# Kernel optimization log

Measured on AMD Instinct MI355X. Metric: run time of the kernel, lower is better.

Reference implementation:

```python
import jax, jax.numpy as jnp
import numpy as np

N_NODES = 100000
FEAT = 256
EMBED = 128
K = 10          # sampled neighbors per node (num_sample)
E = 4096        # edge batch
NUM_CLASSES = 2


def setup_inputs() -> dict:
    key = jax.random.key(0)
    ks = jax.random.split(key, 6)
    edges = jax.random.randint(ks[0], (E, 2), 0, N_NODES)
    neigh_idx = jax.random.randint(ks[1], (N_NODES, K), 0, N_NODES)
    features = jax.random.normal(ks[2], (N_NODES, FEAT), dtype=jnp.float32)
    W1 = jax.random.normal(ks[3], (EMBED, FEAT), dtype=jnp.float32) * (FEAT ** -0.5)
    W2 = jax.random.normal(ks[4], (EMBED, EMBED), dtype=jnp.float32) * (EMBED ** -0.5)
    Wc = jax.random.normal(ks[5], (NUM_CLASSES, EMBED), dtype=jnp.float32) * (EMBED ** -0.5)
    return {"edges": edges, "neigh_idx": neigh_idx, "features": features,
            "W1": W1, "W2": W2, "Wc": Wc}


def reference(edges, neigh_idx, features, W1, W2, Wc):
    # 2-layer GraphSage-style encoder (gcn mean aggregation), batched over E edges.
    idx2 = neigh_idx[edges]              # [E,2,K]   1-hop neighbors of edge endpoints
    idx1 = neigh_idx[idx2]               # [E,2,K,K] 2-hop neighbors
    # layer 1: mean of raw features over 2-hop neighbor sets, then linear + relu
    f1 = jnp.mean(features[idx1], axis=3)                 # [E,2,K,FEAT]
    h1 = jax.nn.relu(jnp.einsum('epkf,df->epkd', f1, W1)) # [E,2,K,EMBED]
    # layer 2: mean over 1-hop neighbors, then linear (last encoder: no relu)
    h1m = jnp.mean(h1, axis=2)                            # [E,2,EMBED]
    h2 = jnp.einsum('epd,gd->epg', h1m, W2)               # [E,2,EMBED]
    # edge pooling ('mean'): average the two endpoint embeddings
    pooled = 0.5 * (h2[:, 0] + h2[:, 1])                  # [E,EMBED]
    # classifier: weight.mm(embeds).t()
    return pooled @ Wc.T                                  # [E,NUM_CLASSES]
```

## Files before the change

### kernel.cpp

```cpp
#include <hip/hip_runtime.h>
#include <hip/hip_bf16.h>


typedef __bf16 bf16x8 __attribute__((ext_vector_type(8)));
typedef float f32x4 __attribute__((ext_vector_type(4)));

#define FEAT 256
#define EMB  128
#define KNB  10

__device__ inline unsigned short f2b(float f) {
  unsigned int u = __float_as_uint(f);
  unsigned int r = (u + 0x7fffu + ((u >> 16) & 1u)) >> 16;
  return (unsigned short)r;
}
__device__ inline float b2f(unsigned short s) {
  return __uint_as_float(((unsigned int)s) << 16);
}


__global__ void cvt_w1(const float* __restrict__ W1, unsigned short* __restrict__ w1b) {
  int i = blockIdx.x * 256 + threadIdx.x;
  if (i < EMB * FEAT) w1b[i] = f2b(W1[i]);
}

__global__ void make_m2(const float* __restrict__ W2, const float* __restrict__ Wc,
                        float* __restrict__ M2) {
  int t = threadIdx.x;
  int c = t >> 7, d = t & 127;
  float s = 0.f;
  for (int g = 0; g < EMB; ++g) s += Wc[c * EMB + g] * W2[g * EMB + d];
  M2[t] = s;
}


__global__ __launch_bounds__(512, 4) void gemm_z(
    const float* __restrict__ feat, const unsigned short* __restrict__ w1b,
    unsigned short* __restrict__ z, int M) {
  __shared__ unsigned short As[64][FEAT + 8];

  const int wid  = threadIdx.x >> 6;
  const int lane = threadIdx.x & 63;
  const int m0   = blockIdx.x * 64;

  bf16x8 bfrag[8];
  {
    const int col = wid * 16 + (lane & 15);
    const int kof = (lane >> 4) * 8;
#pragma unroll
    for (int kk = 0; kk < 8; ++kk)
      bfrag[kk] = *reinterpret_cast<const bf16x8*>(&w1b[col * FEAT + kk * 32 + kof]);
  }

  const float4* f4 = reinterpret_cast<const float4*>(feat);
  for (int i = threadIdx.x; i < 64 * 64; i += 512) {
    int r = i >> 6, c4 = i & 63;
    int row = m0 + r;
    float4 v = make_float4(0.f, 0.f, 0.f, 0.f);
    if (row < M) v = f4[(size_t)row * 64 + c4];
    ushort4 b;
    b.x = f2b(v.x); b.y = f2b(v.y); b.z = f2b(v.z); b.w = f2b(v.w);
    *reinterpret_cast<ushort4*>(&As[r][c4 * 4]) = b;
  }
  __syncthreads();

  f32x4 acc[4] = {};
  const int arow = lane & 15;
  const int kof  = (lane >> 4) * 8;
#pragma unroll
  for (int mt = 0; mt < 4; ++mt) {
#pragma unroll
    for (int kk = 0; kk < 8; ++kk) {
      bf16x8 a = *reinterpret_cast<const bf16x8*>(&As[mt * 16 + arow][kk * 32 + kof]);
      acc[mt] = __builtin_amdgcn_mfma_f32_16x16x32_bf16(a, bfrag[kk], acc[mt], 0, 0, 0);
    }
  }

  const int col = wid * 16 + (lane & 15);
#pragma unroll
  for (int mt = 0; mt < 4; ++mt) {
    int rbase = m0 + mt * 16 + (lane >> 4) * 4;
#pragma unroll
    for (int r = 0; r < 4; ++r) {
      int row = rbase + r;
      if (row < M) z[(size_t)row * EMB + col] = f2b(acc[mt][r]);
    }
  }
}


__global__ __launch_bounds__(128) void aggregate(
    const int* __restrict__ edges, const int* __restrict__ nidx,
    const unsigned short* __restrict__ z, const float* __restrict__ M2,
    float* __restrict__ out, int E) {
  __shared__ int s_idx1[2 * KNB * KNB];
  __shared__ int s_idx2[2 * KNB];
  __shared__ float pm[EMB];

  const int e = blockIdx.x;
  const int t = threadIdx.x;

  if (t < 2 * KNB) {
    int v = edges[e * 2 + t / KNB];
    s_idx2[t] = nidx[(size_t)v * KNB + (t % KNB)];
  }
  __syncthreads();
  for (int i = t; i < 2 * KNB * KNB; i += 128)
    s_idx1[i] = nidx[(size_t)s_idx2[i / KNB] * KNB + (i % KNB)];
  __syncthreads();

  float pooled = 0.f;
#pragma unroll
  for (int p = 0; p < 2; ++p) {
    float h = 0.f;
#pragma unroll
    for (int k = 0; k < KNB; ++k) {
      float a = 0.f;
#pragma unroll
      for (int j = 0; j < KNB; ++j) {
        int u = s_idx1[p * 100 + k * KNB + j];
        a += b2f(z[(size_t)u * EMB + t]);
      }
      h += fmaxf(a * 0.1f, 0.f);
    }
    pooled += h * 0.1f * 0.5f;
  }

  pm[t] = pooled;
  __syncthreads();
  if (t < 64) {
    float s0 = pm[t] * M2[t]       + pm[t + 64] * M2[t + 64];
    float s1 = pm[t] * M2[EMB + t] + pm[t + 64] * M2[EMB + t + 64];
#pragma unroll
    for (int off = 32; off > 0; off >>= 1) {
      s0 += __shfl_down(s0, off);
      s1 += __shfl_down(s1, off);
    }
    if (t == 0) { out[e * 2 + 0] = s0; out[e * 2 + 1] = s1; }
  }
}


extern "C" void kernel_launch(void* const* d_in, const int* in_sizes, int n_in,
                              void* d_out, int out_size, void* d_ws, size_t ws_size,
                              hipStream_t stream) {
  const int*   edges = (const int*)d_in[0];
  const int*   nidx  = (const int*)d_in[1];
  const float* feat  = (const float*)d_in[2];
  const float* W1    = (const float*)d_in[3];
  const float* W2    = (const float*)d_in[4];
  const float* Wc    = (const float*)d_in[5];
  float* out = (float*)d_out;

  const int N = in_sizes[2] / FEAT;
  const int E = in_sizes[0] / 2;

  char* ws = (char*)d_ws;
  unsigned short* z   = (unsigned short*)ws;
  size_t zbytes = (size_t)N * EMB * sizeof(unsigned short);
  unsigned short* w1b = (unsigned short*)(ws + zbytes);
  float* M2 = (float*)(ws + zbytes + (size_t)EMB * FEAT * sizeof(unsigned short));

  cvt_w1 <<<(EMB * FEAT + 255) / 256, 256, 0, stream>>>(W1, w1b);
  make_m2<<<1, 256, 0, stream>>>(W2, Wc, M2);
  gemm_z <<<(N + 63) / 64, 512, 0, stream>>>(feat, w1b, z, N);
  aggregate<<<E, 128, 0, stream>>>(edges, nidx, z, M2, out, E);
}
```

Measured before the change: 209.3 us.

## Merge setup kernels, enlarge GEMM row tile, split aggregation by endpoint per wave

The W1 conversion and M2 precompute kernels are merged into one launch, removing a kernel launch. The feature-projection GEMM tile grows from 64 to 128 rows per block, so each block reuses its register-held W1 fragments over more rows, at the cost of more LDS and fewer blocks. The aggregation kernel now gives each wave one edge endpoint and has each lane load two bf16 values with a single 32-bit gather, which halves the number of gather instructions.

```diff
diff --git a/kernel.cpp b/kernel.cpp
--- a/kernel.cpp
+++ b/kernel.cpp
@@ -8,6 +8,7 @@
 #define FEAT 256
 #define EMB  128
 #define KNB  10
+#define BM   128
 
 __device__ inline unsigned short f2b(float f) {
   unsigned int u = __float_as_uint(f);
@@ -19,29 +20,30 @@
 }
 
 
-__global__ void cvt_w1(const float* __restrict__ W1, unsigned short* __restrict__ w1b) {
-  int i = blockIdx.x * 256 + threadIdx.x;
-  if (i < EMB * FEAT) w1b[i] = f2b(W1[i]);
-}
-
-__global__ void make_m2(const float* __restrict__ W2, const float* __restrict__ Wc,
-                        float* __restrict__ M2) {
-  int t = threadIdx.x;
-  int c = t >> 7, d = t & 127;
-  float s = 0.f;
-  for (int g = 0; g < EMB; ++g) s += Wc[c * EMB + g] * W2[g * EMB + d];
-  M2[t] = s;
+__global__ void setup(const float* __restrict__ W1, const float* __restrict__ W2,
+                      const float* __restrict__ Wc,
+                      unsigned short* __restrict__ w1b, float* __restrict__ M2) {
+  const int b = blockIdx.x;
+  if (b < 128) {
+    int i = b * 256 + threadIdx.x;
+    w1b[i] = f2b(W1[i]);
+  } else {
+    int t = threadIdx.x, c = t >> 7, d = t & 127;
+    float s = 0.f;
+    for (int g = 0; g < EMB; ++g) s += Wc[c * EMB + g] * W2[g * EMB + d];
+    M2[t] = s;
+  }
 }
 
 
 __global__ __launch_bounds__(512, 4) void gemm_z(
     const float* __restrict__ feat, const unsigned short* __restrict__ w1b,
     unsigned short* __restrict__ z, int M) {
-  __shared__ unsigned short As[64][FEAT + 8];
+  __shared__ unsigned short As[BM][FEAT + 8];
 
   const int wid  = threadIdx.x >> 6;
   const int lane = threadIdx.x & 63;
-  const int m0   = blockIdx.x * 64;
+  const int m0   = blockIdx.x * BM;
 
   bf16x8 bfrag[8];
   {
@@ -53,22 +55,22 @@
   }
 
   const float4* f4 = reinterpret_cast<const float4*>(feat);
-  for (int i = threadIdx.x; i < 64 * 64; i += 512) {
+  for (int i = threadIdx.x; i < BM * 64; i += 512) {
     int r = i >> 6, c4 = i & 63;
     int row = m0 + r;
     float4 v = make_float4(0.f, 0.f, 0.f, 0.f);
     if (row < M) v = f4[(size_t)row * 64 + c4];
-    ushort4 b;
-    b.x = f2b(v.x); b.y = f2b(v.y); b.z = f2b(v.z); b.w = f2b(v.w);
-    *reinterpret_cast<ushort4*>(&As[r][c4 * 4]) = b;
+    ushort4 bq;
+    bq.x = f2b(v.x); bq.y = f2b(v.y); bq.z = f2b(v.z); bq.w = f2b(v.w);
+    *reinterpret_cast<ushort4*>(&As[r][c4 * 4]) = bq;
   }
   __syncthreads();
 
-  f32x4 acc[4] = {};
+  f32x4 acc[BM / 16] = {};
   const int arow = lane & 15;
   const int kof  = (lane >> 4) * 8;
 #pragma unroll
-  for (int mt = 0; mt < 4; ++mt) {
+  for (int mt = 0; mt < BM / 16; ++mt) {
 #pragma unroll
     for (int kk = 0; kk < 8; ++kk) {
       bf16x8 a = *reinterpret_cast<const bf16x8*>(&As[mt * 16 + arow][kk * 32 + kof]);
@@ -78,7 +80,7 @@
 
   const int col = wid * 16 + (lane & 15);
 #pragma unroll
-  for (int mt = 0; mt < 4; ++mt) {
+  for (int mt = 0; mt < BM / 16; ++mt) {
     int rbase = m0 + mt * 16 + (lane >> 4) * 4;
 #pragma unroll
     for (int r = 0; r < 4; ++r) {
@@ -93,50 +95,57 @@
     const int* __restrict__ edges, const int* __restrict__ nidx,
     const unsigned short* __restrict__ z, const float* __restrict__ M2,
     float* __restrict__ out, int E) {
-  __shared__ int s_idx1[2 * KNB * KNB];
-  __shared__ int s_idx2[2 * KNB];
-  __shared__ float pm[EMB];
+  __shared__ int   s_idx2[2][KNB];
+  __shared__ int   s_idx1[2][KNB * KNB];
+  __shared__ float s_pm[2][EMB];
 
   const int e = blockIdx.x;
   const int t = threadIdx.x;
+  const int w = t >> 6;
+  const int l = t & 63;
 
   if (t < 2 * KNB) {
-    int v = edges[e * 2 + t / KNB];
-    s_idx2[t] = nidx[(size_t)v * KNB + (t % KNB)];
+    int p = t / KNB, k = t % KNB;
+    int v = edges[e * 2 + p];
+    s_idx2[p][k] = nidx[(size_t)v * KNB + k];
   }
   __syncthreads();
-  for (int i = t; i < 2 * KNB * KNB; i += 128)
-    s_idx1[i] = nidx[(size_t)s_idx2[i / KNB] * KNB + (i % KNB)];
+  for (int i = t; i < 2 * KNB * KNB; i += 128) {
+    int p = i / 100, r = i % 100;
+    s_idx1[p][r] = nidx[(size_t)s_idx2[p][r / KNB] * KNB + (r % KNB)];
+  }
   __syncthreads();
 
-  float pooled = 0.f;
+  float pooled0 = 0.f, pooled1 = 0.f;
 #pragma unroll
-  for (int p = 0; p < 2; ++p) {
-    float h = 0.f;
+  for (int k = 0; k < KNB; ++k) {
+    float a0 = 0.f, a1 = 0.f;
 #pragma unroll
-    for (int k = 0; k < KNB; ++k) {
-      float a = 0.f;
-#pragma unroll
-      for (int j = 0; j < KNB; ++j) {
-        int u = s_idx1[p * 100 + k * KNB + j];
-        a += b2f(z[(size_t)u * EMB + t]);
-      }
-      h += fmaxf(a * 0.1f, 0.f);
+    for (int j = 0; j < KNB; ++j) {
+      int u = s_idx1[w][k * KNB + j];
+      unsigned int q = *reinterpret_cast<const unsigned int*>(&z[(size_t)u * EMB + 2 * l]);
+      a0 += b2f((unsigned short)(q & 0xffffu));
+      a1 += b2f((unsigned short)(q >> 16));
     }
-    pooled += h * 0.1f * 0.5f;
+    pooled0 += fmaxf(a0 * 0.1f, 0.f);
+    pooled1 += fmaxf(a1 * 0.1f, 0.f);
   }
+  s_pm[w][2 * l]     = pooled0 * 0.1f;
+  s_pm[w][2 * l + 1] = pooled1 * 0.1f;
+  __syncthreads();
 
-  pm[t] = pooled;
-  __syncthreads();
-  if (t < 64) {
-    float s0 = pm[t] * M2[t]       + pm[t + 64] * M2[t + 64];
-    float s1 = pm[t] * M2[EMB + t] + pm[t + 64] * M2[EMB + t + 64];
+  if (w == 0) {
+    int d0 = 2 * l, d1 = 2 * l + 1;
+    float p0 = 0.5f * (s_pm[0][d0] + s_pm[1][d0]);
+    float p1 = 0.5f * (s_pm[0][d1] + s_pm[1][d1]);
+    float s0 = p0 * M2[d0]       + p1 * M2[d1];
+    float s1 = p0 * M2[EMB + d0] + p1 * M2[EMB + d1];
 #pragma unroll
     for (int off = 32; off > 0; off >>= 1) {
       s0 += __shfl_down(s0, off);
       s1 += __shfl_down(s1, off);
     }
-    if (t == 0) { out[e * 2 + 0] = s0; out[e * 2 + 1] = s1; }
+    if (l == 0) { out[e * 2 + 0] = s0; out[e * 2 + 1] = s1; }
   }
 }
 
@@ -161,8 +170,7 @@
   unsigned short* w1b = (unsigned short*)(ws + zbytes);
   float* M2 = (float*)(ws + zbytes + (size_t)EMB * FEAT * sizeof(unsigned short));
 
-  cvt_w1 <<<(EMB * FEAT + 255) / 256, 256, 0, stream>>>(W1, w1b);
-  make_m2<<<1, 256, 0, stream>>>(W2, Wc, M2);
-  gemm_z <<<(N + 63) / 64, 512, 0, stream>>>(feat, w1b, z, N);
+  setup  <<<129, 256, 0, stream>>>(W1, W2, Wc, w1b, M2);
+  gemm_z <<<(N + BM - 1) / BM, 512, 0, stream>>>(feat, w1b, z, N);
   aggregate<<<E, 128, 0, stream>>>(edges, nidx, z, M2, out, E);
 }
```

Measured after the change: 214.7 us. +2.5%, slower.
